# Performance work log

Measured on AMD Instinct MI355X. Metric: run time of the kernel, lower is better.

The kernel has to match this reference:

```python
import jax, jax.numpy as jnp
import numpy as np

N, E, G, D, L, T = 50000, 100000, 2000, 300, 5, 10
NUM_ATOM, NUM_CHIR, NUM_BOND, NUM_DIR = 120, 3, 6, 3


def setup_inputs() -> dict:
    key = jax.random.key(0)
    ks = jax.random.split(key, 24)
    s = 1.0 / np.sqrt(D)
    inp = {
        'x': jnp.stack([jax.random.randint(ks[0], (N,), 0, NUM_ATOM),
                        jax.random.randint(ks[1], (N,), 0, NUM_CHIR)], axis=1),
        'edge_index': jax.random.randint(ks[2], (2, E), 0, N),
        'edge_attr': jnp.stack([jax.random.randint(ks[3], (E,), 0, 4),
                                jax.random.randint(ks[4], (E,), 0, NUM_DIR)], axis=1),
        'batch': jnp.sort(jax.random.randint(ks[5], (N,), 0, G)),
        'x1': jnp.stack([jax.random.randint(ks[6], (N,), 0, NUM_ATOM),
                         jax.random.randint(ks[7], (N,), 0, NUM_CHIR)], axis=1),
        'edge_index1': jax.random.randint(ks[8], (2, E), 0, N),
        'edge_attr1': jnp.stack([jax.random.randint(ks[9], (E,), 0, 4),
                                 jax.random.randint(ks[10], (E,), 0, NUM_DIR)], axis=1),
        'batch1': jnp.sort(jax.random.randint(ks[11], (N,), 0, G)),
        'xemb1': jax.random.normal(ks[12], (NUM_ATOM, D)) * s,
        'xemb2': jax.random.normal(ks[13], (NUM_CHIR, D)) * s,
        'eemb1': jax.random.normal(ks[14], (L, NUM_BOND, D)) * s,
        'eemb2': jax.random.normal(ks[15], (L, NUM_DIR, D)) * s,
        'W1': jax.random.normal(ks[16], (L, D, 2 * D)) * s,
        'b1': jnp.zeros((L, 2 * D)),
        'W2': jax.random.normal(ks[17], (L, 2 * D, D)) * (1.0 / np.sqrt(2 * D)),
        'b2': jnp.zeros((L, D)),
        'gamma': jnp.ones((L, D)),
        'beta': jnp.zeros((L, D)),
        'predW': jax.random.normal(ks[18], (D, T)) * s,
        'predb': jnp.zeros((T,)),
    }
    return inp


def _gnn(xi, ei, ea, xemb1, xemb2, eemb1, eemb2, W1, b1, W2, b2, gamma, beta):
    n = xi.shape[0]
    h = xemb1[xi[:, 0]] + xemb2[xi[:, 1]]  # [N, D]
    loop = jnp.arange(n)
    src = jnp.concatenate([ei[0], loop])
    dst = jnp.concatenate([ei[1], loop])
    # self-loop edge attr = [4, 0]
    sl = jnp.concatenate([jnp.full((n, 1), 4, ea.dtype), jnp.zeros((n, 1), ea.dtype)], axis=1)
    eaf = jnp.concatenate([ea, sl], axis=0)
    for l in range(L):
        eemb = eemb1[l][eaf[:, 0]] + eemb2[l][eaf[:, 1]]     # [E+N, D]
        msg = h[src] + eemb                                   # gather
        agg = jax.ops.segment_sum(msg, dst, num_segments=n)   # scatter-add
        h2 = jax.nn.relu(agg @ W1[l] + b1[l]) @ W2[l] + b2[l] # GIN MLP
        mu = h2.mean(axis=0)
        var = ((h2 - mu) ** 2).mean(axis=0)                   # batchnorm (train stats)
        h2 = gamma[l] * (h2 - mu) * jax.lax.rsqrt(var + 1e-5) + beta[l]
        if l < L - 1:
            h2 = jax.nn.relu(h2)
        h = h2
    return h  # JK='last'


def _mean_pool(node_rep, batch):
    s = jax.ops.segment_sum(node_rep, batch, num_segments=G)
    cnt = jax.ops.segment_sum(jnp.ones((node_rep.shape[0],), node_rep.dtype), batch, num_segments=G)
    return s / jnp.maximum(cnt, 1.0)[:, None]


def reference(x, edge_index, edge_attr, batch, x1, edge_index1, edge_attr1, batch1,
              xemb1, xemb2, eemb1, eemb2, W1, b1, W2, b2, gamma, beta, predW, predb):
    node_rep = _gnn(x, edge_index, edge_attr, xemb1, xemb2, eemb1, eemb2, W1, b1, W2, b2, gamma, beta)
    node_rep1 = _gnn(x1, edge_index1, edge_attr1, xemb1, xemb2, eemb1, eemb2, W1, b1, W2, b2, gamma, beta)
    graph_rep = _mean_pool(node_rep, batch)
    graph_rep1 = _mean_pool(node_rep1, batch1)
    pred = graph_rep @ predW + predb
    pred1 = graph_rep1 @ predW + predb
    return (pred, graph_rep, node_rep, pred1, graph_rep1, node_rep1)
```

## Files before the change

kernel.cpp:

```cpp
#include <hip/hip_runtime.h>
#include <hip/hip_bf16.h>

typedef unsigned short ushort_t;
typedef short v8s __attribute__((ext_vector_type(8)));
typedef unsigned short v8u __attribute__((ext_vector_type(8)));
typedef unsigned short v4u __attribute__((ext_vector_type(4)));
typedef float v4f __attribute__((ext_vector_type(4)));

#define N_NODES 50000
#define N_EDGES 100000
#define N_GRAPH 2000
#define DIM     300
#define DIM2    600
#define NLAYER  5
#define NTASK   10
#define D4      75
#define D4P     80

#define LDA  304
#define LDY  608
#define LDAH 320
#define NPAD 50048

#define KB1 40
#define NT1 5
#define KB2 76
#define NT2 3
#define MT_TILES 391

#define AS1 __attribute__((address_space(1)))
#define AS3 __attribute__((address_space(3)))
static __device__ __forceinline__ void gload_lds16(const void* g, void* l) {
    __builtin_amdgcn_global_load_lds((AS1 void*)(g), (AS3 void*)(l), 16, 0, 0);
}

static __device__ __forceinline__ ushort_t f2bf(float f) {
    unsigned int u;
    __builtin_memcpy(&u, &f, 4);
    unsigned int lsb = (u >> 16) & 1u;
    u += 0x7fffu + lsb;
    return (ushort_t)(u >> 16);
}
static __device__ __forceinline__ void split2(float f, ushort_t& h, ushort_t& l) {
    unsigned int u;
    __builtin_memcpy(&u, &f, 4);
    h = (ushort_t)(u >> 16);
    unsigned int um = u & 0xFFFF0000u;
    float hf;
    __builtin_memcpy(&hf, &um, 4);
    float lf = f - hf;
    unsigned int ul;
    __builtin_memcpy(&ul, &lf, 4);
    l = (ushort_t)(ul >> 16);
}

static __device__ __forceinline__ int swz_wgid(int orig, int nwg) {
    int xcd = orig & 7;
    int seq = orig >> 3;
    int q = nwg >> 3, r = nwg & 7;
    int base = (xcd < r) ? xcd * (q + 1) : r * (q + 1) + (xcd - r) * q;
    return base + seq;
}

__global__ void k_embed_init(const int* __restrict__ x,
                             const float* __restrict__ xe1,
                             const float* __restrict__ xe2,
                             float* __restrict__ h) {
    int tid = blockIdx.x * blockDim.x + threadIdx.x;
    if (tid >= N_NODES * D4) return;
    int node = tid / D4;
    int d0 = (tid % D4) * 4;
    int i0 = x[node * 2 + 0];
    int i1 = x[node * 2 + 1];
    float4 a = *(const float4*)(xe1 + (size_t)i0 * DIM + d0);
    float4 b = *(const float4*)(xe2 + (size_t)i1 * DIM + d0);
    float4 o;
    o.x = a.x + b.x; o.y = a.y + b.y; o.z = a.z + b.z; o.w = a.w + b.w;
    *(float4*)(h + (size_t)node * LDA + d0) = o;
}

__global__ void k_deg(const int* __restrict__ ei, int* __restrict__ deg) {
    int e = blockIdx.x * blockDim.x + threadIdx.x;
    if (e >= N_EDGES) return;
    atomicAdd(&deg[ei[N_EDGES + e]], 1);
}

__global__ void k_scan1(const int* __restrict__ deg, int* __restrict__ excl,
                        int* __restrict__ blksum) {
    __shared__ int s[256];
    int i = blockIdx.x * 256 + threadIdx.x;
    int v = (i < N_NODES) ? deg[i] : 0;
    s[threadIdx.x] = v;
    __syncthreads();
#pragma unroll
    for (int o = 1; o < 256; o <<= 1) {
        int t = (threadIdx.x >= o) ? s[threadIdx.x - o] : 0;
        __syncthreads();
        s[threadIdx.x] += t;
        __syncthreads();
    }
    if (i < N_NODES) excl[i] = s[threadIdx.x] - v;
    if (threadIdx.x == 255) blksum[blockIdx.x] = s[255];
}

__global__ void k_scan2(int* __restrict__ blksum, int* __restrict__ blkoff, int nblk) {
    __shared__ int s[256];
    int v = (threadIdx.x < nblk) ? blksum[threadIdx.x] : 0;
    s[threadIdx.x] = v;
    __syncthreads();
#pragma unroll
    for (int o = 1; o < 256; o <<= 1) {
        int t = (threadIdx.x >= o) ? s[threadIdx.x - o] : 0;
        __syncthreads();
        s[threadIdx.x] += t;
        __syncthreads();
    }
    if (threadIdx.x < nblk) blkoff[threadIdx.x] = s[threadIdx.x] - v;
}

__global__ void k_scan3(const int* __restrict__ excl, const int* __restrict__ blkoff,
                        int* __restrict__ rowptr, int* __restrict__ fillptr) {
    int i = blockIdx.x * blockDim.x + threadIdx.x;
    if (i > N_NODES) return;
    int v = (i < N_NODES) ? (excl[i] + blkoff[i >> 8]) : N_EDGES;
    rowptr[i] = v;
    if (i < N_NODES) fillptr[i] = v;
}

__global__ void k_fill(const int* __restrict__ ei, const int* __restrict__ ea,
                       int* __restrict__ fillptr,
                       int* __restrict__ csrc, int* __restrict__ cea) {
    int e = blockIdx.x * blockDim.x + threadIdx.x;
    if (e >= N_EDGES) return;
    int dst = ei[N_EDGES + e];
    int pos = atomicAdd(&fillptr[dst], 1);
    csrc[pos] = ei[e];
    cea[pos] = (ea[2 * e + 0] << 16) | ea[2 * e + 1];
}

template <bool BN>
__global__ void k_gather_agg(const int* __restrict__ rowptr,
                             const int* __restrict__ csrc,
                             const int* __restrict__ cea,
                             const float* __restrict__ hin,
                             const float* __restrict__ ee1,
                             const float* __restrict__ ee2,
                             const float* __restrict__ ee1sl,
                             const float* __restrict__ ee2sl,
                             const float* __restrict__ bnmean,
                             const float* __restrict__ bnrstd,
                             const float* __restrict__ bngam,
                             const float* __restrict__ bnbet,
                             ushort_t* __restrict__ aghi,
                             ushort_t* __restrict__ aglo) {
    int tid = blockIdx.x * blockDim.x + threadIdx.x;
    if (tid >= N_NODES * D4P) return;
    int node = tid / D4P;
    int c = tid % D4P;
    if (c >= D4) {
        v4u z = (v4u){0, 0, 0, 0};
        *(v4u*)(aghi + (size_t)node * LDAH + c * 4) = z;
        *(v4u*)(aglo + (size_t)node * LDAH + c * 4) = z;
        return;
    }
    int d0 = c * 4;
    float4 m4, r4, g4, b4;
    if (BN) {
        m4 = *(const float4*)(bnmean + d0);
        r4 = *(const float4*)(bnrstd + d0);
        g4 = *(const float4*)(bngam + d0);
        b4 = *(const float4*)(bnbet + d0);
    }
    auto bn4 = [&](float4 v) -> float4 {
        if (BN) {
            v.x = fmaxf((v.x - m4.x) * r4.x * g4.x + b4.x, 0.f);
            v.y = fmaxf((v.y - m4.y) * r4.y * g4.y + b4.y, 0.f);
            v.z = fmaxf((v.z - m4.z) * r4.z * g4.z + b4.z, 0.f);
            v.w = fmaxf((v.w - m4.w) * r4.w * g4.w + b4.w, 0.f);
        }
        return v;
    };
    float4 a = bn4(*(const float4*)(hin + (size_t)node * LDA + d0));
    float4 e1 = *(const float4*)(ee1sl + d0);
    float4 e2 = *(const float4*)(ee2sl + d0);
    a.x += e1.x + e2.x; a.y += e1.y + e2.y; a.z += e1.z + e2.z; a.w += e1.w + e2.w;
    int p0 = rowptr[node], p1 = rowptr[node + 1];
    for (int p = p0; p < p1; ++p) {
        int src = csrc[p];
        int pk = cea[p];
        int a0 = pk >> 16, a1 = pk & 0xFFFF;
        float4 hv = bn4(*(const float4*)(hin + (size_t)src * LDA + d0));
        float4 f1 = *(const float4*)(ee1 + (size_t)a0 * DIM + d0);
        float4 f2 = *(const float4*)(ee2 + (size_t)a1 * DIM + d0);
        a.x += hv.x + f1.x + f2.x;
        a.y += hv.y + f1.y + f2.y;
        a.z += hv.z + f1.z + f2.z;
        a.w += hv.w + f1.w + f2.w;
    }
    float av[4] = {a.x, a.y, a.z, a.w};
    v4u hh, ll;
#pragma unroll
    for (int i = 0; i < 4; ++i) {
        ushort_t uh, ul;
        split2(av[i], uh, ul);
        hh[i] = uh;
        ll[i] = ul;
    }
    *(v4u*)(aghi + (size_t)node * LDAH + d0) = hh;
    *(v4u*)(aglo + (size_t)node * LDAH + d0) = ll;
}

__global__ void k_pack_w(const float* __restrict__ W,
                         ushort_t* __restrict__ hi,
                         ushort_t* __restrict__ lo,
                         int K, int N, int KBv, int NTv, int total) {
    int idx = blockIdx.x * blockDim.x + threadIdx.x;
    if (idx >= total) return;
    int j = idx & 7;
    int n = (idx >> 3) & 127;
    int tmp = idx >> 10;
    int kb = tmp % KBv; tmp /= KBv;
    int nt = tmp % NTv;
    int l = tmp / NTv;
    int k = kb * 8 + j;
    int ng = nt * 128 + n;
    float v = 0.f;
    if (k < K && ng < N) v = W[((size_t)l * K + k) * N + ng];
    ushort_t h, lw;
    split2(v, h, lw);
    hi[idx] = h;
    lo[idx] = lw;
}

template <bool RELU, bool SPLITA, bool BNSTAT, typename OT>
__global__ __launch_bounds__(256) void k_gemm_mfma(
        const ushort_t* __restrict__ Ahi,
        const ushort_t* __restrict__ Alo,
        const ushort_t* __restrict__ Bhi,
        const ushort_t* __restrict__ Blo,
        const float* __restrict__ bias,
        OT* __restrict__ C,
        double* __restrict__ bnsum,
        double* __restrict__ bnsq,
        int M, int N, int Ksteps, int KBv, int NTv, int nwg,
        int lda, int ldc, int ncap) {
    alignas(16) __shared__ ushort_t sAhi[8192];
    alignas(16) __shared__ ushort_t sBhi[8192];

    const int wgid = swz_wgid(blockIdx.x, nwg);
    const int nt = wgid % NTv;
    const int mt = wgid / NTv;
    const int t = threadIdx.x;

    const int w = t >> 6;
    const int lane = t & 63;
    const int wm = w >> 1;
    const int wn = w & 1;
    const int quad = lane >> 4;
    const int lr = lane & 15;

    v4f acc[4][4];
#pragma unroll
    for (int i = 0; i < 4; ++i)
#pragma unroll
        for (int j = 0; j < 4; ++j) acc[i][j] = (v4f){0.f, 0.f, 0.f, 0.f};

    auto stage = [&](int buf, int ks) {
        const int kk = ks * 32;
        const int bo = buf * 4096;
        const size_t base = ((size_t)nt * KBv + ks * 4) * 1024;
#pragma unroll
        for (int p = 0; p < 2; ++p) {
            int o = p * 2048 + t * 8;
            gload_lds16(Bhi + base + o, &sBhi[bo + o]);
        }
#pragma unroll
        for (int p = 0; p < 2; ++p) {
            int cidx = p * 256 + t;
            int kb = cidx >> 7;
            int m = cidx & 127;
            size_t go = (size_t)(mt * 128 + m) * lda + kk + kb * 8;
            gload_lds16(Ahi + go, &sAhi[bo + cidx * 8]);
        }
    };

    stage(0, 0);
    __syncthreads();
    int cur = 0;
    for (int ks = 0; ks < Ksteps; ++ks) {
        const int kk = ks * 32;
        const int bo = cur * 4096;
        v8s a_hi[4], b_hi[4], a_lo[4], b_lo[4];
#pragma unroll
        for (int s = 0; s < 4; ++s) {
            a_hi[s] = *(const v8s*)&sAhi[bo + quad * 1024 + (wm * 64 + s * 16 + lr) * 8];
            b_hi[s] = *(const v8s*)&sBhi[bo + quad * 1024 + (wn * 64 + s * 16 + lr) * 8];
        }
#pragma unroll
        for (int s = 0; s < 4; ++s) {
            b_lo[s] = *(const v8s*)(Blo + ((size_t)(nt * KBv + ks * 4 + quad)) * 1024 +
                                    (wn * 64 + s * 16 + lr) * 8);
            if (SPLITA)
                a_lo[s] = *(const v8s*)(Alo + (size_t)(mt * 128 + wm * 64 + s * 16 + lr) * lda +
                                        kk + quad * 8);
        }
        if (ks + 1 < Ksteps) stage(cur ^ 1, ks + 1);
#pragma unroll
        for (int si = 0; si < 4; ++si)
#pragma unroll
            for (int sj = 0; sj < 4; ++sj)
                acc[si][sj] = __builtin_amdgcn_mfma_f32_16x16x32_bf16(
                    a_hi[si], b_hi[sj], acc[si][sj], 0, 0, 0);
#pragma unroll
        for (int si = 0; si < 4; ++si)
#pragma unroll
            for (int sj = 0; sj < 4; ++sj)
                acc[si][sj] = __builtin_amdgcn_mfma_f32_16x16x32_bf16(
                    a_hi[si], b_lo[sj], acc[si][sj], 0, 0, 0);
        if (SPLITA) {
#pragma unroll
            for (int si = 0; si < 4; ++si)
#pragma unroll
                for (int sj = 0; sj < 4; ++sj)
                    acc[si][sj] = __builtin_amdgcn_mfma_f32_16x16x32_bf16(
                        a_lo[si], b_hi[sj], acc[si][sj], 0, 0, 0);
        }
        __syncthreads();
        cur ^= 1;
    }

    float bsum[4], bsq[4];
    if (BNSTAT) {
#pragma unroll
        for (int sj = 0; sj < 4; ++sj) { bsum[sj] = 0.f; bsq[sj] = 0.f; }
    }
#pragma unroll
    for (int sj = 0; sj < 4; ++sj) {
        int col = nt * 128 + wn * 64 + sj * 16 + lr;
        if (col >= ncap) continue;
        float bv = (col < N) ? bias[col] : 0.f;
#pragma unroll
        for (int si = 0; si < 4; ++si) {
#pragma unroll
            for (int r = 0; r < 4; ++r) {
                size_t row = (size_t)mt * 128 + wm * 64 + si * 16 + quad * 4 + r;
                float v = acc[si][sj][r] + bv;
                if (RELU) v = fmaxf(v, 0.f);
                if (BNSTAT && row < (size_t)M) { bsum[sj] += v; bsq[sj] += v * v; }
                if (sizeof(OT) == 2)
                    ((ushort_t*)C)[row * ldc + col] = f2bf(v);
                else
                    ((float*)C)[row * ldc + col] = v;
            }
        }
    }
    if (BNSTAT) {
        float* sred = (float*)sBhi;
#pragma unroll
        for (int sj = 0; sj < 4; ++sj) {
            bsum[sj] += __shfl_xor(bsum[sj], 16);
            bsum[sj] += __shfl_xor(bsum[sj], 32);
            bsq[sj]  += __shfl_xor(bsq[sj], 16);
            bsq[sj]  += __shfl_xor(bsq[sj], 32);
        }
        if (quad == 0) {
#pragma unroll
            for (int sj = 0; sj < 4; ++sj) {
                int idx = wm * 128 + wn * 64 + sj * 16 + lr;
                sred[idx] = bsum[sj];
                sred[256 + idx] = bsq[sj];
            }
        }
        __syncthreads();
        if (t < 128) {
            float s = sred[t] + sred[128 + t];
            float q = sred[256 + t] + sred[256 + 128 + t];
            int col = nt * 128 + t;
            if (col < N) {
                atomicAdd(&bnsum[col], (double)s);
                atomicAdd(&bnsq[col], (double)q);
            }
        }
    }
}

__global__ void k_bn_finalize(const double* __restrict__ sum,
                              const double* __restrict__ sumsq,
                              float* __restrict__ mean,
                              float* __restrict__ rstd) {
    int d = threadIdx.x;
    if (d >= DIM) return;
    double mu = sum[d] / (double)N_NODES;
    double var = sumsq[d] / (double)N_NODES - mu * mu;
    if (var < 0.0) var = 0.0;
    mean[d] = (float)mu;
    rstd[d] = (float)(1.0 / sqrt(var + 1e-5));
}

__global__ __launch_bounds__(256) void k_bn_pool(const float* __restrict__ h2,
                                                 const int* __restrict__ batch,
                                                 const float* __restrict__ mean,
                                                 const float* __restrict__ rstd,
                                                 const float* __restrict__ gam,
                                                 const float* __restrict__ bet,
                                                 float* __restrict__ nodeout,
                                                 float* __restrict__ pool,
                                                 float* __restrict__ gout) {
    __shared__ float4 s[3][D4];
    const int g = blockIdx.x;
    int lo = 0, hi = N_NODES;
    while (lo < hi) {
        int m = (lo + hi) >> 1;
        if (batch[m] < g) lo = m + 1; else hi = m;
    }
    const int p0 = lo;
    hi = N_NODES;
    while (lo < hi) {
        int m = (lo + hi) >> 1;
        if (batch[m] < g + 1) lo = m + 1; else hi = m;
    }
    const int p1 = lo;

    const int t = threadIdx.x;
    if (t < 3 * D4) {
        const int c = t % D4;
        const int rc = t / D4;
        const int d0 = c * 4;
        float4 m4 = *(const float4*)(mean + d0);
        float4 r4 = *(const float4*)(rstd + d0);
        float4 g4 = *(const float4*)(gam + d0);
        float4 b4 = *(const float4*)(bet + d0);
        float4 acc = {0.f, 0.f, 0.f, 0.f};
        for (int r = p0 + rc; r < p1; r += 3) {
            float4 v = *(const float4*)(h2 + (size_t)r * LDA + d0);
            v.x = (v.x - m4.x) * r4.x * g4.x + b4.x;
            v.y = (v.y - m4.y) * r4.y * g4.y + b4.y;
            v.z = (v.z - m4.z) * r4.z * g4.z + b4.z;
            v.w = (v.w - m4.w) * r4.w * g4.w + b4.w;
            *(float4*)(nodeout + (size_t)r * DIM + d0) = v;
            acc.x += v.x; acc.y += v.y; acc.z += v.z; acc.w += v.w;
        }
        s[rc][c] = acc;
    }
    __syncthreads();
    if (t < D4) {
        float4 a = s[0][t], b = s[1][t], c = s[2][t];
        const float inv = 1.0f / fmaxf((float)(p1 - p0), 1.0f);
        float4 r;
        r.x = (a.x + b.x + c.x) * inv;
        r.y = (a.y + b.y + c.y) * inv;
        r.z = (a.z + b.z + c.z) * inv;
        r.w = (a.w + b.w + c.w) * inv;
        *(float4*)(pool + (size_t)g * DIM + t * 4) = r;
        *(float4*)(gout + (size_t)g * DIM + t * 4) = r;
    }
}

__global__ void k_pred(const float* __restrict__ pool,
                       const float* __restrict__ predW,
                       const float* __restrict__ predb,
                       float* __restrict__ out) {
    int tid = blockIdx.x * blockDim.x + threadIdx.x;
    if (tid >= N_GRAPH * NTASK) return;
    int g = tid / NTASK;
    int tt = tid % NTASK;
    float s = predb[tt];
    const float* pr = pool + (size_t)g * DIM;
    for (int k = 0; k < DIM; ++k) s += pr[k] * predW[k * NTASK + tt];
    out[(size_t)g * NTASK + tt] = s;
}

static inline int cdiv(long long a, long long b) { return (int)((a + b - 1) / b); }

extern "C" void kernel_launch(void* const* d_in, const int* in_sizes, int n_in,
                              void* d_out, int out_size, void* d_ws, size_t ws_size,
                              hipStream_t stream) {
    const int* x    = (const int*)d_in[0];
    const int* ei   = (const int*)d_in[1];
    const int* ea   = (const int*)d_in[2];
    const int* bat  = (const int*)d_in[3];
    const int* x1   = (const int*)d_in[4];
    const int* ei1  = (const int*)d_in[5];
    const int* ea1  = (const int*)d_in[6];
    const int* bat1 = (const int*)d_in[7];
    const float* xemb1 = (const float*)d_in[8];
    const float* xemb2 = (const float*)d_in[9];
    const float* eemb1 = (const float*)d_in[10];
    const float* eemb2 = (const float*)d_in[11];
    const float* W1    = (const float*)d_in[12];
    const float* b1    = (const float*)d_in[13];
    const float* W2    = (const float*)d_in[14];
    const float* b2    = (const float*)d_in[15];
    const float* gamma = (const float*)d_in[16];
    const float* beta  = (const float*)d_in[17];
    const float* predW = (const float*)d_in[18];
    const float* predb = (const float*)d_in[19];
    float* out = (float*)d_out;

    char* ws = (char*)d_ws;
    size_t off = 0;
    auto take = [&](size_t bytes) -> char* {
        char* p = ws + off;
        off += (bytes + 255) & ~(size_t)255;
        return p;
    };
    const size_t BUFSZ = (size_t)NPAD * LDAH * 2 * 2;
    char* bufA = take(BUFSZ);
    char* bufB = take(BUFSZ);
    float* pool   = (float*)take((size_t)N_GRAPH * DIM * 4);
    double* bnsum = (double*)take(DIM * 8 * 2);
    double* bnsq  = bnsum + DIM;
    float* bnmean = (float*)take(DIM * 4 * 2);
    float* bnrstd = bnmean + DIM;
    const size_t W1P = (size_t)NLAYER * NT1 * KB1 * 1024;
    const size_t W2P = (size_t)NLAYER * NT2 * KB2 * 1024;
    ushort_t* w1hi = (ushort_t*)take(W1P * 2);
    ushort_t* w1lo = (ushort_t*)take(W1P * 2);
    ushort_t* w2hi = (ushort_t*)take(W2P * 2);
    ushort_t* w2lo = (ushort_t*)take(W2P * 2);
    int* deg     = (int*)take(N_NODES * 4);
    int* excl    = (int*)take(N_NODES * 4);
    int* blksum  = (int*)take(256 * 4);
    int* blkoff  = (int*)take(256 * 4);
    int* fillptr = (int*)take(N_NODES * 4);
    int* rowptr0 = (int*)take((N_NODES + 1) * 4);
    int* csrc0   = (int*)take(N_EDGES * 4);
    int* cea0    = (int*)take(N_EDGES * 4);
    int* rowptr1 = (int*)take((N_NODES + 1) * 4);
    int* csrc1   = (int*)take(N_EDGES * 4);
    int* cea1    = (int*)take(N_EDGES * 4);
    (void)ws_size; (void)in_sizes; (void)n_in; (void)out_size;

    const int TB = 256;
    const int gN75 = cdiv((long long)N_NODES * D4, TB);
    const int gN80 = cdiv((long long)N_NODES * D4P, TB);
    const int gE   = cdiv(N_EDGES, TB);
    const int gScan = cdiv(N_NODES, TB);
    const int gScan3 = cdiv(N_NODES + 1, TB);
    const int NWG1 = NT1 * MT_TILES;
    const int NWG2 = NT2 * MT_TILES;

    k_pack_w<<<cdiv((long long)W1P, TB), TB, 0, stream>>>(W1, w1hi, w1lo, DIM, DIM2, KB1, NT1, (int)W1P);
    k_pack_w<<<cdiv((long long)W2P, TB), TB, 0, stream>>>(W2, w2hi, w2lo, DIM2, DIM, KB2, NT2, (int)W2P);

    auto build_csr = [&](const int* eip, const int* eap, int* rowptr, int* csrc, int* cea) {
        hipMemsetAsync(deg, 0, N_NODES * 4, stream);
        k_deg<<<gE, TB, 0, stream>>>(eip, deg);
        k_scan1<<<gScan, TB, 0, stream>>>(deg, excl, blksum);
        k_scan2<<<1, 256, 0, stream>>>(blksum, blkoff, gScan);
        k_scan3<<<gScan3, TB, 0, stream>>>(excl, blkoff, rowptr, fillptr);
        k_fill<<<gE, TB, 0, stream>>>(eip, eap, fillptr, csrc, cea);
    };
    build_csr(ei, ea, rowptr0, csrc0, cea0);
    build_csr(ei1, ea1, rowptr1, csrc1, cea1);

    auto run_gnn = [&](const int* xp, const int* batp,
                       const int* rowptr, const int* csrc, const int* cea,
                       float* out_pred, float* out_graph, float* out_node) {
        k_embed_init<<<gN75, TB, 0, stream>>>(xp, xemb1, xemb2, (float*)bufA);
        for (int l = 0; l < NLAYER; ++l) {
            char* pb = (l & 1) ? bufA : bufB;
            char* yb = (l & 1) ? bufB : bufA;
            ushort_t* aghi = (ushort_t*)pb;
            ushort_t* aglo = aghi + (size_t)NPAD * LDAH;
            const float* gin = (const float*)yb;
            ushort_t* yv = (ushort_t*)yb;
            float* h2v = (float*)pb;
            const float* ee1l = eemb1 + (size_t)l * 6 * DIM;
            const float* ee2l = eemb2 + (size_t)l * 3 * DIM;
            if (l == 0)
                k_gather_agg<false><<<gN80, TB, 0, stream>>>(
                    rowptr, csrc, cea, gin, ee1l, ee2l, ee1l + 4 * DIM, ee2l,
                    nullptr, nullptr, nullptr, nullptr, aghi, aglo);
            else
                k_gather_agg<true><<<gN80, TB, 0, stream>>>(
                    rowptr, csrc, cea, gin, ee1l, ee2l, ee1l + 4 * DIM, ee2l,
                    bnmean, bnrstd, gamma + (size_t)(l - 1) * DIM, beta + (size_t)(l - 1) * DIM,
                    aghi, aglo);
            k_gemm_mfma<true, true, false, ushort_t>
                <<<NWG1, TB, 0, stream>>>(
                    aghi, aglo,
                    w1hi + (size_t)l * NT1 * KB1 * 1024, w1lo + (size_t)l * NT1 * KB1 * 1024,
                    b1 + (size_t)l * DIM2, yv, nullptr, nullptr,
                    N_NODES, DIM2, 10, KB1, NT1, NWG1, LDAH, LDY, LDY);
            hipMemsetAsync(bnsum, 0, DIM * 8 * 2, stream);
            k_gemm_mfma<false, false, true, float>
                <<<NWG2, TB, 0, stream>>>(
                    yv, yv,
                    w2hi + (size_t)l * NT2 * KB2 * 1024, w2lo + (size_t)l * NT2 * KB2 * 1024,
                    b2 + (size_t)l * DIM, h2v, bnsum, bnsq,
                    N_NODES, DIM, 19, KB2, NT2, NWG2, LDY, LDA, LDA);
            k_bn_finalize<<<1, 512, 0, stream>>>(bnsum, bnsq, bnmean, bnrstd);
        }
        k_bn_pool<<<N_GRAPH, TB, 0, stream>>>(
            (const float*)bufB, batp, bnmean, bnrstd,
            gamma + (size_t)(NLAYER - 1) * DIM, beta + (size_t)(NLAYER - 1) * DIM,
            out_node, pool, out_graph);
        k_pred<<<cdiv((long long)N_GRAPH * NTASK, TB), TB, 0, stream>>>(pool, predW, predb, out_pred);
    };

    const size_t GT = (size_t)N_GRAPH * NTASK;
    const size_t GD = (size_t)N_GRAPH * DIM;
    const size_t ND = (size_t)N_NODES * DIM;
    run_gnn(x, bat, rowptr0, csrc0, cea0, out, out + GT, out + GT + GD);
    run_gnn(x1, bat1, rowptr1, csrc1, cea1,
            out + GT + GD + ND, out + 2 * GT + GD + ND, out + 2 * GT + 2 * GD + ND);
}
```

Baseline: 2.147 ms.

## Stage low-precision A/B splits through LDS and issue prefetch before compute

New measurement: 2.167 ms. About the same (+0.9%).

```diff
diff --git a/kernel.cpp b/kernel.cpp
--- a/kernel.cpp
+++ b/kernel.cpp
@@ -245,7 +245,9 @@
         int M, int N, int Ksteps, int KBv, int NTv, int nwg,
         int lda, int ldc, int ncap) {
     alignas(16) __shared__ ushort_t sAhi[8192];
+    alignas(16) __shared__ ushort_t sAlo[SPLITA ? 8192 : 16];
     alignas(16) __shared__ ushort_t sBhi[8192];
+    alignas(16) __shared__ ushort_t sBlo[8192];
 
     const int wgid = swz_wgid(blockIdx.x, nwg);
     const int nt = wgid % NTv;
@@ -273,6 +275,7 @@
         for (int p = 0; p < 2; ++p) {
             int o = p * 2048 + t * 8;
             gload_lds16(Bhi + base + o, &sBhi[bo + o]);
+            gload_lds16(Blo + base + o, &sBlo[bo + o]);
         }
 #pragma unroll
         for (int p = 0; p < 2; ++p) {
@@ -281,6 +284,7 @@
             int m = cidx & 127;
             size_t go = (size_t)(mt * 128 + m) * lda + kk + kb * 8;
             gload_lds16(Ahi + go, &sAhi[bo + cidx * 8]);
+            if (SPLITA) gload_lds16(Alo + go, &sAlo[bo + cidx * 8]);
         }
     };
 
@@ -288,42 +292,29 @@
     __syncthreads();
     int cur = 0;
     for (int ks = 0; ks < Ksteps; ++ks) {
-        const int kk = ks * 32;
+        if (ks + 1 < Ksteps) stage(cur ^ 1, ks + 1);
         const int bo = cur * 4096;
-        v8s a_hi[4], b_hi[4], a_lo[4], b_lo[4];
+        v8s a_hi[4], a_lo[4];
 #pragma unroll
         for (int s = 0; s < 4; ++s) {
             a_hi[s] = *(const v8s*)&sAhi[bo + quad * 1024 + (wm * 64 + s * 16 + lr) * 8];
-            b_hi[s] = *(const v8s*)&sBhi[bo + quad * 1024 + (wn * 64 + s * 16 + lr) * 8];
-        }
-#pragma unroll
-        for (int s = 0; s < 4; ++s) {
-            b_lo[s] = *(const v8s*)(Blo + ((size_t)(nt * KBv + ks * 4 + quad)) * 1024 +
-                                    (wn * 64 + s * 16 + lr) * 8);
             if (SPLITA)
-                a_lo[s] = *(const v8s*)(Alo + (size_t)(mt * 128 + wm * 64 + s * 16 + lr) * lda +
-                                        kk + quad * 8);
-        }
-        if (ks + 1 < Ksteps) stage(cur ^ 1, ks + 1);
-#pragma unroll
-        for (int si = 0; si < 4; ++si)
-#pragma unroll
-            for (int sj = 0; sj < 4; ++sj)
+                a_lo[s] = *(const v8s*)&sAlo[bo + quad * 1024 + (wm * 64 + s * 16 + lr) * 8];
+        }
+#pragma unroll
+        for (int sj = 0; sj < 4; ++sj) {
+            v8s bh = *(const v8s*)&sBhi[bo + quad * 1024 + (wn * 64 + sj * 16 + lr) * 8];
+            v8s bl = *(const v8s*)&sBlo[bo + quad * 1024 + (wn * 64 + sj * 16 + lr) * 8];
+#pragma unroll
+            for (int si = 0; si < 4; ++si) {
                 acc[si][sj] = __builtin_amdgcn_mfma_f32_16x16x32_bf16(
-                    a_hi[si], b_hi[sj], acc[si][sj], 0, 0, 0);
-#pragma unroll
-        for (int si = 0; si < 4; ++si)
-#pragma unroll
-            for (int sj = 0; sj < 4; ++sj)
+                    a_hi[si], bh, acc[si][sj], 0, 0, 0);
                 acc[si][sj] = __builtin_amdgcn_mfma_f32_16x16x32_bf16(
-                    a_hi[si], b_lo[sj], acc[si][sj], 0, 0, 0);
-        if (SPLITA) {
-#pragma unroll
-            for (int si = 0; si < 4; ++si)
-#pragma unroll
-                for (int sj = 0; sj < 4; ++sj)
+                    a_hi[si], bl, acc[si][sj], 0, 0, 0);
+                if (SPLITA)
                     acc[si][sj] = __builtin_amdgcn_mfma_f32_16x16x32_bf16(
-                        a_lo[si], b_hi[sj], acc[si][sj], 0, 0, 0);
+                        a_lo[si], bh, acc[si][sj], 0, 0, 0);
+            }
         }
         __syncthreads();
         cur ^= 1;
```
